# Kernel tuning notes

Measured on AMD Instinct MI355X. Metric: run time of the kernel, lower is better.

The kernel has to match this reference:

```python
import jax, jax.numpy as jnp
import numpy as np


def setup_inputs() -> dict:
    key = jax.random.key(0)
    k1, k2, k3 = jax.random.split(key, 3)
    N, Q, K, E = 8, 2048, 2048, 512
    query = jax.random.normal(k1, (N, Q, E), dtype=jnp.float32)
    keys = jax.random.normal(k2, (N, K, E), dtype=jnp.float32)
    values = jax.random.normal(k3, (N, K, E), dtype=jnp.float32)
    return {"query": query, "keys": keys, "values": values}


def reference(query, keys, values):
    # energy: [N, Q, K] -- note: NO 1/sqrt(d) scaling, matching the original
    energy = jnp.einsum('nqe,nke->nqk', query, keys)
    attention = jax.nn.softmax(energy, axis=-1)
    out = jnp.einsum('nqk,nke->nqe', attention, values)
    return out
```

## Files before the change

### kernel.cpp

```cpp
#include <hip/hip_runtime.h>
#include <stdint.h>


typedef __attribute__((ext_vector_type(8))) _Float16 half8;
typedef __attribute__((ext_vector_type(2))) _Float16 half2;
typedef __attribute__((ext_vector_type(4))) float    floatx4;

#define NBATCH 8
#define SEQ    2048
#define EDIM   512
static constexpr size_t NE = (size_t)NBATCH * SEQ * EDIM;

__device__ __forceinline__ void block_sync_lds() {
  asm volatile("s_waitcnt lgkmcnt(0)\n\ts_barrier" ::: "memory");
}

__device__ __forceinline__ half8 cvt8(float4 a, float4 b) {
  half8 h;
  h[0] = (_Float16)a.x; h[1] = (_Float16)a.y; h[2] = (_Float16)a.z; h[3] = (_Float16)a.w;
  h[4] = (_Float16)b.x; h[5] = (_Float16)b.y; h[6] = (_Float16)b.z; h[7] = (_Float16)b.w;
  return h;
}


__global__ void make_frags(const float* __restrict__ q, const float* __restrict__ k,
                           const float* __restrict__ v,
                           _Float16* __restrict__ qf, _Float16* __restrict__ kf,
                           _Float16* __restrict__ vf) {
  __shared__ float lds[32][260];
  const int tid = threadIdx.x;
  const int seg = blockIdx.x >> 9;
  const int b   = blockIdx.x & 511;
  const int n = b >> 6, kt = b & 63;
  const float* src = (seg == 0 ? q : seg == 1 ? k : v) + ((size_t)n * SEQ + kt * 32) * EDIM;

  if (seg < 2) {
    _Float16* dst = (seg == 0 ? qf : kf) + ((size_t)(n * 128 + kt * 2) * 16) * 512;
#pragma unroll
    for (int eh = 0; eh < 2; eh++) {
      if (eh) __syncthreads();
#pragma unroll
      for (int i = 0; i < 8; i++) {
        int c = i * 256 + tid;
        int row = c >> 6, col4 = c & 63;
        float4 x = *reinterpret_cast<const float4*>(src + (size_t)row * EDIM + eh * 256 + col4 * 4);
        *reinterpret_cast<float4*>(&lds[row][col4 * 4]) = x;
      }
      __syncthreads();
#pragma unroll
      for (int i = 0; i < 4; i++) {
        int fl = i * 256 + tid;
        int lane = fl & 63, idx = fl >> 6;
        int est_l = idx & 7, rt_l = idx >> 3;
        int m15 = lane & 15, q4 = lane >> 4;
        const float* p = &lds[rt_l * 16 + m15][est_l * 32 + q4 * 8];
        float4 a = *reinterpret_cast<const float4*>(p);
        float4 bb = *reinterpret_cast<const float4*>(p + 4);
        *reinterpret_cast<half8*>(dst + ((size_t)(rt_l * 16 + eh * 8 + est_l)) * 512 + lane * 8) =
            cvt8(a, bb);
      }
    }
  } else {
    _Float16* dst = vf + ((size_t)(n * 64 + kt) * 32) * 512;
#pragma unroll
    for (int eh = 0; eh < 2; eh++) {
      if (eh) __syncthreads();
#pragma unroll
      for (int i = 0; i < 8; i++) {
        int c = i * 256 + tid;
        int row = c >> 6, col4 = c & 63;
        float4 x = *reinterpret_cast<const float4*>(src + (size_t)row * EDIM + eh * 256 + col4 * 4);
        *reinterpret_cast<float4*>(&lds[row][col4 * 4]) = x;
      }
      __syncthreads();
#pragma unroll
      for (int i = 0; i < 4; i++) {
        int fl = i * 256 + tid;
        int etl = fl >> 6, ln = fl & 63;
        int m15 = ln & 15, q4 = ln >> 4;
        int e_local = etl * 16 + m15;
        half8 h;
#pragma unroll
        for (int j = 0; j < 8; j++) h[j] = (_Float16)lds[q4 * 8 + j][e_local];
        *reinterpret_cast<half8*>(dst + ((size_t)eh * 1024 + fl) * 8) = h;
      }
    }
  }
}

__launch_bounds__(512, 4)
__global__ void attn_fused(const _Float16* __restrict__ qf, const _Float16* __restrict__ kf,
                           const _Float16* __restrict__ vf, float* __restrict__ out) {
  __shared__ float    s_part[4][32][36];
  __shared__ _Float16 p_lds[32][40];
  __shared__ float    m_lds[32], l_lds[32], a_lds[32];

  const int tid  = threadIdx.x;
  const int lane = tid & 63, w = tid >> 6;
  const int m15  = lane & 15, q4 = lane >> 4;
  const int n    = blockIdx.x & 7, qt = blockIdx.x >> 3;
  const int ks   = w & 1, es = w >> 1;

  if (tid < 32) { m_lds[tid] = -3.0e38f; l_lds[tid] = 0.0f; }

  half8 qfr[2][4];
  {
    const uint32_t qbase = ((uint32_t)(n * 128 + qt * 2) * 16 + es * 4) * 512 + (uint32_t)lane * 8;
#pragma unroll
    for (int s = 0; s < 2; s++)
#pragma unroll
      for (int i = 0; i < 4; i++)
        qfr[s][i] = *reinterpret_cast<const half8*>(qf + qbase + (uint32_t)(s * 16 + i) * 512);
  }

  floatx4 oacc[2][4];
#pragma unroll
  for (int s = 0; s < 2; s++)
#pragma unroll
    for (int j = 0; j < 4; j++) oacc[s][j] = (floatx4){0.f, 0.f, 0.f, 0.f};

  uint32_t koff = ((uint32_t)(n * 128 + ks) * 16 + es * 4) * 512 + (uint32_t)lane * 8;
  uint32_t voff = ((uint32_t)(n * 64) * 32 + w * 4) * 512 + (uint32_t)lane * 8;

  block_sync_lds();

  for (int t = 0; t < 64; t++) {
    half8 kfr[4];
#pragma unroll
    for (int i = 0; i < 4; i++)
      kfr[i] = *reinterpret_cast<const half8*>(kf + koff + (uint32_t)i * 512);
    koff += 16384;

    floatx4 sacc[2];
    sacc[0] = (floatx4){0.f, 0.f, 0.f, 0.f};
    sacc[1] = (floatx4){0.f, 0.f, 0.f, 0.f};
    __builtin_amdgcn_s_setprio(1);
#pragma unroll
    for (int i = 0; i < 4; i++) {
      sacc[0] = __builtin_amdgcn_mfma_f32_16x16x32_f16(qfr[0][i], kfr[i], sacc[0], 0, 0, 0);
      sacc[1] = __builtin_amdgcn_mfma_f32_16x16x32_f16(qfr[1][i], kfr[i], sacc[1], 0, 0, 0);
    }
    __builtin_amdgcn_s_setprio(0);

    half8 vfr[4];
#pragma unroll
    for (int j = 0; j < 4; j++)
      vfr[j] = *reinterpret_cast<const half8*>(vf + voff + (uint32_t)j * 512);
    voff += 16384;

#pragma unroll
    for (int s = 0; s < 2; s++)
#pragma unroll
      for (int r = 0; r < 4; r++)
        s_part[es][s * 16 + q4 * 4 + r][ks * 16 + m15] = sacc[s][r];
    block_sync_lds();

    {
      const int r = tid >> 4, sub = tid & 15, c = sub * 2;
      float svx = s_part[0][r][c],     svy = s_part[0][r][c + 1];
#pragma unroll
      for (int pl = 1; pl < 4; pl++) { svx += s_part[pl][r][c]; svy += s_part[pl][r][c + 1]; }
      float mx = fmaxf(svx, svy);
#pragma unroll
      for (int o = 1; o < 16; o <<= 1) mx = fmaxf(mx, __shfl_xor(mx, o));
      const float mo = m_lds[r];
      const float mn = fmaxf(mo, mx);
      const float px = __expf(svx - mn), py = __expf(svy - mn);
      float rs = px + py;
#pragma unroll
      for (int o = 1; o < 16; o <<= 1) rs += __shfl_xor(rs, o);
      if (sub == 0) {
        const float al = __expf(mo - mn);
        a_lds[r] = al; m_lds[r] = mn; l_lds[r] = l_lds[r] * al + rs;
      }
      half2 ph; ph[0] = (_Float16)px; ph[1] = (_Float16)py;
      *reinterpret_cast<half2*>(&p_lds[r][c]) = ph;
    }
    block_sync_lds();

    half8 pfr[2];
    pfr[0] = *reinterpret_cast<const half8*>(&p_lds[m15][q4 * 8]);
    pfr[1] = *reinterpret_cast<const half8*>(&p_lds[16 + m15][q4 * 8]);
    {
      floatx4 al0 = *reinterpret_cast<floatx4*>(&a_lds[q4 * 4]);
      floatx4 al1 = *reinterpret_cast<floatx4*>(&a_lds[16 + q4 * 4]);
#pragma unroll
      for (int j = 0; j < 4; j++) { oacc[0][j] *= al0; oacc[1][j] *= al1; }
    }
    __builtin_amdgcn_s_setprio(1);
#pragma unroll
    for (int j = 0; j < 4; j++) {
      oacc[0][j] = __builtin_amdgcn_mfma_f32_16x16x32_f16(pfr[0], vfr[j], oacc[0][j], 0, 0, 0);
      oacc[1][j] = __builtin_amdgcn_mfma_f32_16x16x32_f16(pfr[1], vfr[j], oacc[1][j], 0, 0, 0);
    }
    __builtin_amdgcn_s_setprio(0);
  }

  const int q0 = qt * 32;
#pragma unroll
  for (int s = 0; s < 2; s++) {
    floatx4 lv = *reinterpret_cast<floatx4*>(&l_lds[s * 16 + q4 * 4]);
#pragma unroll
    for (int j = 0; j < 4; j++) {
      const int col = (w * 4 + j) * 16 + m15;
#pragma unroll
      for (int r = 0; r < 4; r++) {
        const int row = s * 16 + q4 * 4 + r;
        out[((size_t)n * SEQ + q0 + row) * EDIM + col] = oacc[s][j][r] / lv[r];
      }
    }
  }
}

__global__ void attn_fallback(const float* __restrict__ q, const float* __restrict__ k,
                              const float* __restrict__ v, float* __restrict__ out) {
  __shared__ float qrow[EDIM];
  __shared__ float sc[SEQ];
  __shared__ float red[16];
  const int tid = threadIdx.x;
  const int n = blockIdx.x >> 11, qi = blockIdx.x & 2047;
  const int wv = tid >> 6, ln = tid & 63;
  const float* qp = q + ((size_t)n * SEQ + qi) * EDIM;
  for (int e = tid; e < EDIM; e += 256) qrow[e] = qp[e];
  __syncthreads();
  for (int kk = wv; kk < SEQ; kk += 4) {
    const float* kp = k + ((size_t)n * SEQ + kk) * EDIM;
    float s = 0.f;
    for (int e = ln; e < EDIM; e += 64) s = fmaf(qrow[e], kp[e], s);
    for (int o = 32; o > 0; o >>= 1) s += __shfl_down(s, o);
    if (ln == 0) sc[kk] = s;
  }
  __syncthreads();
  float mx = -3.0e38f;
  for (int kk = tid; kk < SEQ; kk += 256) mx = fmaxf(mx, sc[kk]);
  for (int o = 32; o > 0; o >>= 1) mx = fmaxf(mx, __shfl_down(mx, o));
  if (ln == 0) red[wv] = mx;
  __syncthreads();
  if (tid == 0) {
    float m2 = red[0];
    for (int i = 1; i < 4; i++) m2 = fmaxf(m2, red[i]);
    red[8] = m2;
  }
  __syncthreads();
  const float m = red[8];
  float ls = 0.f;
  for (int kk = tid; kk < SEQ; kk += 256) { float p = __expf(sc[kk] - m); sc[kk] = p; ls += p; }
  for (int o = 32; o > 0; o >>= 1) ls += __shfl_down(ls, o);
  if (ln == 0) red[wv] = ls;
  __syncthreads();
  if (tid == 0) { red[9] = red[0] + red[1] + red[2] + red[3]; }
  __syncthreads();
  const float linv = 1.f / red[9];
  for (int e = tid; e < EDIM; e += 256) {
    float acc = 0.f;
    const float* vp = v + ((size_t)n * SEQ) * EDIM + e;
    for (int kk = 0; kk < SEQ; kk++) acc = fmaf(sc[kk], vp[(size_t)kk * EDIM], acc);
    out[((size_t)n * SEQ + qi) * EDIM + e] = acc * linv;
  }
}

extern "C" void kernel_launch(void* const* d_in, const int* in_sizes, int n_in,
                              void* d_out, int out_size, void* d_ws, size_t ws_size,
                              hipStream_t stream) {
  const float* q = (const float*)d_in[0];
  const float* k = (const float*)d_in[1];
  const float* v = (const float*)d_in[2];
  float* out = (float*)d_out;
  const size_t need = 3 * NE * sizeof(_Float16);
  if (ws_size >= need) {
    _Float16* qf = (_Float16*)d_ws;
    _Float16* kf = qf + NE;
    _Float16* vf = kf + NE;
    make_frags<<<1536, 256, 0, stream>>>(q, k, v, qf, kf, vf);
    attn_fused<<<512, 512, 0, stream>>>(qf, kf, vf, out);
  } else {
    attn_fallback<<<16384, 256, 0, stream>>>(q, k, v, out);
  }
}
```

Before: 239.1 us.

## Convert Q in-kernel instead of prepass, and prefetch next K fragments

New measurement: 234.9 us. Within noise of the previous version (-1.8%).

```diff
diff --git a/kernel.cpp b/kernel.cpp
--- a/kernel.cpp
+++ b/kernel.cpp
@@ -23,19 +23,17 @@
 }
 
 
-__global__ void make_frags(const float* __restrict__ q, const float* __restrict__ k,
-                           const float* __restrict__ v,
-                           _Float16* __restrict__ qf, _Float16* __restrict__ kf,
-                           _Float16* __restrict__ vf) {
+__global__ void make_frags(const float* __restrict__ k, const float* __restrict__ v,
+                           _Float16* __restrict__ kf, _Float16* __restrict__ vf) {
   __shared__ float lds[32][260];
   const int tid = threadIdx.x;
   const int seg = blockIdx.x >> 9;
   const int b   = blockIdx.x & 511;
   const int n = b >> 6, kt = b & 63;
-  const float* src = (seg == 0 ? q : seg == 1 ? k : v) + ((size_t)n * SEQ + kt * 32) * EDIM;
-
-  if (seg < 2) {
-    _Float16* dst = (seg == 0 ? qf : kf) + ((size_t)(n * 128 + kt * 2) * 16) * 512;
+  const float* src = (seg == 0 ? k : v) + ((size_t)n * SEQ + kt * 32) * EDIM;
+
+  if (seg == 0) {
+    _Float16* dst = kf + ((size_t)(n * 128 + kt * 2) * 16) * 512;
 #pragma unroll
     for (int eh = 0; eh < 2; eh++) {
       if (eh) __syncthreads();
@@ -89,7 +87,7 @@
 }
 
 __launch_bounds__(512, 4)
-__global__ void attn_fused(const _Float16* __restrict__ qf, const _Float16* __restrict__ kf,
+__global__ void attn_fused(const float* __restrict__ q, const _Float16* __restrict__ kf,
                            const _Float16* __restrict__ vf, float* __restrict__ out) {
   __shared__ float    s_part[4][32][36];
   __shared__ _Float16 p_lds[32][40];
@@ -105,12 +103,16 @@
 
   half8 qfr[2][4];
   {
-    const uint32_t qbase = ((uint32_t)(n * 128 + qt * 2) * 16 + es * 4) * 512 + (uint32_t)lane * 8;
+    const float* qb = q + ((size_t)n * SEQ + qt * 32 + m15) * EDIM + es * 128 + q4 * 8;
 #pragma unroll
     for (int s = 0; s < 2; s++)
 #pragma unroll
-      for (int i = 0; i < 4; i++)
-        qfr[s][i] = *reinterpret_cast<const half8*>(qf + qbase + (uint32_t)(s * 16 + i) * 512);
+      for (int i = 0; i < 4; i++) {
+        const float* src = qb + (size_t)s * 16 * EDIM + i * 32;
+        float4 a = *reinterpret_cast<const float4*>(src);
+        float4 b = *reinterpret_cast<const float4*>(src + 4);
+        qfr[s][i] = cvt8(a, b);
+      }
   }
 
   floatx4 oacc[2][4];
@@ -122,25 +124,31 @@
   uint32_t koff = ((uint32_t)(n * 128 + ks) * 16 + es * 4) * 512 + (uint32_t)lane * 8;
   uint32_t voff = ((uint32_t)(n * 64) * 32 + w * 4) * 512 + (uint32_t)lane * 8;
 
+  half8 kcur[4];
+#pragma unroll
+  for (int i = 0; i < 4; i++)
+    kcur[i] = *reinterpret_cast<const half8*>(kf + koff + (uint32_t)i * 512);
+  koff += 16384;
+
   block_sync_lds();
 
   for (int t = 0; t < 64; t++) {
-    half8 kfr[4];
-#pragma unroll
-    for (int i = 0; i < 4; i++)
-      kfr[i] = *reinterpret_cast<const half8*>(kf + koff + (uint32_t)i * 512);
-    koff += 16384;
-
     floatx4 sacc[2];
     sacc[0] = (floatx4){0.f, 0.f, 0.f, 0.f};
     sacc[1] = (floatx4){0.f, 0.f, 0.f, 0.f};
     __builtin_amdgcn_s_setprio(1);
 #pragma unroll
     for (int i = 0; i < 4; i++) {
-      sacc[0] = __builtin_amdgcn_mfma_f32_16x16x32_f16(qfr[0][i], kfr[i], sacc[0], 0, 0, 0);
-      sacc[1] = __builtin_amdgcn_mfma_f32_16x16x32_f16(qfr[1][i], kfr[i], sacc[1], 0, 0, 0);
+      sacc[0] = __builtin_amdgcn_mfma_f32_16x16x32_f16(qfr[0][i], kcur[i], sacc[0], 0, 0, 0);
+      sacc[1] = __builtin_amdgcn_mfma_f32_16x16x32_f16(qfr[1][i], kcur[i], sacc[1], 0, 0, 0);
     }
     __builtin_amdgcn_s_setprio(0);
+
+    half8 knxt[4];
+#pragma unroll
+    for (int i = 0; i < 4; i++)
+      knxt[i] = *reinterpret_cast<const half8*>(kf + koff + (uint32_t)i * 512);
+    koff += 16384;
 
     half8 vfr[4];
 #pragma unroll
@@ -194,6 +202,9 @@
       oacc[1][j] = __builtin_amdgcn_mfma_f32_16x16x32_f16(pfr[1], vfr[j], oacc[1][j], 0, 0, 0);
     }
     __builtin_amdgcn_s_setprio(0);
+
+#pragma unroll
+    for (int i = 0; i < 4; i++) kcur[i] = knxt[i];
   }
 
   const int q0 = qt * 32;
@@ -266,13 +277,12 @@
   const float* k = (const float*)d_in[1];
   const float* v = (const float*)d_in[2];
   float* out = (float*)d_out;
-  const size_t need = 3 * NE * sizeof(_Float16);
+  const size_t need = 2 * NE * sizeof(_Float16);
   if (ws_size >= need) {
-    _Float16* qf = (_Float16*)d_ws;
-    _Float16* kf = qf + NE;
+    _Float16* kf = (_Float16*)d_ws;
     _Float16* vf = kf + NE;
-    make_frags<<<1536, 256, 0, stream>>>(q, k, v, qf, kf, vf);
-    attn_fused<<<512, 512, 0, stream>>>(qf, kf, vf, out);
+    make_frags<<<1024, 256, 0, stream>>>(k, v, kf, vf);
+    attn_fused<<<512, 512, 0, stream>>>(q, kf, vf, out);
   } else {
     attn_fallback<<<16384, 256, 0, stream>>>(q, k, v, out);
   }
```

## Fuse fragment conversion and attention into one cooperative kernel with grid sync

Applied to the files above, without the earlier changes.

After: 320.5 us. 34.1% more time.

```diff
diff --git a/kernel.cpp b/kernel.cpp
--- a/kernel.cpp
+++ b/kernel.cpp
@@ -1,5 +1,8 @@
 #include <hip/hip_runtime.h>
+#include <hip/hip_cooperative_groups.h>
 #include <stdint.h>
+
+namespace cg = cooperative_groups;
 
 
 typedef __attribute__((ext_vector_type(8))) _Float16 half8;
@@ -22,6 +25,191 @@
   return h;
 }
 
+
+__launch_bounds__(512, 4)
+__global__ void attn_all(const float* __restrict__ q, const float* __restrict__ k,
+                         const float* __restrict__ v,
+                         _Float16* __restrict__ qf, _Float16* __restrict__ kf,
+                         _Float16* __restrict__ vf, float* __restrict__ out) {
+  __shared__ __align__(16) char smem[33280];
+
+  const int tid = threadIdx.x;
+
+  {
+    float (*lds)[260] = reinterpret_cast<float (*)[260]>(smem);
+    const int b = blockIdx.x;
+    const int n = b >> 6, kt = b & 63;
+#pragma unroll 1
+    for (int seg = 0; seg < 3; seg++) {
+      const float* src = (seg == 0 ? q : seg == 1 ? k : v) +
+                         ((size_t)n * SEQ + kt * 32) * EDIM;
+      if (seg) __syncthreads();
+#pragma unroll 1
+      for (int eh = 0; eh < 2; eh++) {
+        if (eh) __syncthreads();
+#pragma unroll
+        for (int i = 0; i < 4; i++) {
+          int c = i * 512 + tid;
+          int row = c >> 6, col4 = c & 63;
+          float4 x = *reinterpret_cast<const float4*>(src + (size_t)row * EDIM + eh * 256 + col4 * 4);
+          *reinterpret_cast<float4*>(&lds[row][col4 * 4]) = x;
+        }
+        __syncthreads();
+        if (seg < 2) {
+          _Float16* dst = (seg == 0 ? qf : kf) + ((size_t)(n * 128 + kt * 2) * 16) * 512;
+#pragma unroll
+          for (int i = 0; i < 2; i++) {
+            int fl = i * 512 + tid;
+            int lane = fl & 63, idx = fl >> 6;
+            int est_l = idx & 7, rt_l = idx >> 3;
+            int m15 = lane & 15, q4 = lane >> 4;
+            const float* p = &lds[rt_l * 16 + m15][est_l * 32 + q4 * 8];
+            float4 a = *reinterpret_cast<const float4*>(p);
+            float4 bb = *reinterpret_cast<const float4*>(p + 4);
+            *reinterpret_cast<half8*>(dst + ((size_t)(rt_l * 16 + eh * 8 + est_l)) * 512 + lane * 8) =
+                cvt8(a, bb);
+          }
+        } else {
+          _Float16* dst = vf + ((size_t)(n * 64 + kt) * 32) * 512;
+#pragma unroll
+          for (int i = 0; i < 2; i++) {
+            int fl = i * 512 + tid;
+            int etl = fl >> 6, ln = fl & 63;
+            int m15 = ln & 15, q4 = ln >> 4;
+            int e_local = etl * 16 + m15;
+            half8 h;
+#pragma unroll
+            for (int j = 0; j < 8; j++) h[j] = (_Float16)lds[q4 * 8 + j][e_local];
+            *reinterpret_cast<half8*>(dst + ((size_t)eh * 1024 + fl) * 8) = h;
+          }
+        }
+      }
+    }
+  }
+
+  cg::this_grid().sync();
+
+  float    (*s_part)[32][36] = reinterpret_cast<float (*)[32][36]>(smem);
+  _Float16 (*p_lds)[40]      = reinterpret_cast<_Float16 (*)[40]>(smem + 18432);
+  float*    m_lds            = reinterpret_cast<float*>(smem + 18432 + 2560);
+  float*    l_lds            = m_lds + 32;
+  float*    a_lds            = m_lds + 64;
+
+  const int lane = tid & 63, w = tid >> 6;
+  const int m15  = lane & 15, q4 = lane >> 4;
+  const int n    = blockIdx.x & 7, qt = blockIdx.x >> 3;
+  const int ks   = w & 1, es = w >> 1;
+
+  if (tid < 32) { m_lds[tid] = -3.0e38f; l_lds[tid] = 0.0f; }
+
+  half8 qfr[2][4];
+  {
+    const uint32_t qbase = ((uint32_t)(n * 128 + qt * 2) * 16 + es * 4) * 512 + (uint32_t)lane * 8;
+#pragma unroll
+    for (int s = 0; s < 2; s++)
+#pragma unroll
+      for (int i = 0; i < 4; i++)
+        qfr[s][i] = *reinterpret_cast<const half8*>(qf + qbase + (uint32_t)(s * 16 + i) * 512);
+  }
+
+  floatx4 oacc[2][4];
+#pragma unroll
+  for (int s = 0; s < 2; s++)
+#pragma unroll
+    for (int j = 0; j < 4; j++) oacc[s][j] = (floatx4){0.f, 0.f, 0.f, 0.f};
+
+  uint32_t koff = ((uint32_t)(n * 128 + ks) * 16 + es * 4) * 512 + (uint32_t)lane * 8;
+  uint32_t voff = ((uint32_t)(n * 64) * 32 + w * 4) * 512 + (uint32_t)lane * 8;
+
+  block_sync_lds();
+
+  for (int t = 0; t < 64; t++) {
+    half8 kfr[4];
+#pragma unroll
+    for (int i = 0; i < 4; i++)
+      kfr[i] = *reinterpret_cast<const half8*>(kf + koff + (uint32_t)i * 512);
+    koff += 16384;
+
+    floatx4 sacc[2];
+    sacc[0] = (floatx4){0.f, 0.f, 0.f, 0.f};
+    sacc[1] = (floatx4){0.f, 0.f, 0.f, 0.f};
+    __builtin_amdgcn_s_setprio(1);
+#pragma unroll
+    for (int i = 0; i < 4; i++) {
+      sacc[0] = __builtin_amdgcn_mfma_f32_16x16x32_f16(qfr[0][i], kfr[i], sacc[0], 0, 0, 0);
+      sacc[1] = __builtin_amdgcn_mfma_f32_16x16x32_f16(qfr[1][i], kfr[i], sacc[1], 0, 0, 0);
+    }
+    __builtin_amdgcn_s_setprio(0);
+
+    half8 vfr[4];
+#pragma unroll
+    for (int j = 0; j < 4; j++)
+      vfr[j] = *reinterpret_cast<const half8*>(vf + voff + (uint32_t)j * 512);
+    voff += 16384;
+
+#pragma unroll
+    for (int s = 0; s < 2; s++)
+#pragma unroll
+      for (int r = 0; r < 4; r++)
+        s_part[es][s * 16 + q4 * 4 + r][ks * 16 + m15] = sacc[s][r];
+    block_sync_lds();
+
+    {
+      const int r = tid >> 4, sub = tid & 15, c = sub * 2;
+      float svx = s_part[0][r][c],     svy = s_part[0][r][c + 1];
+#pragma unroll
+      for (int pl = 1; pl < 4; pl++) { svx += s_part[pl][r][c]; svy += s_part[pl][r][c + 1]; }
+      float mx = fmaxf(svx, svy);
+#pragma unroll
+      for (int o = 1; o < 16; o <<= 1) mx = fmaxf(mx, __shfl_xor(mx, o));
+      const float mo = m_lds[r];
+      const float mn = fmaxf(mo, mx);
+      const float px = __expf(svx - mn), py = __expf(svy - mn);
+      float rs = px + py;
+#pragma unroll
+      for (int o = 1; o < 16; o <<= 1) rs += __shfl_xor(rs, o);
+      if (sub == 0) {
+        const float al = __expf(mo - mn);
+        a_lds[r] = al; m_lds[r] = mn; l_lds[r] = l_lds[r] * al + rs;
+      }
+      half2 ph; ph[0] = (_Float16)px; ph[1] = (_Float16)py;
+      *reinterpret_cast<half2*>(&p_lds[r][c]) = ph;
+    }
+    block_sync_lds();
+
+    half8 pfr[2];
+    pfr[0] = *reinterpret_cast<const half8*>(&p_lds[m15][q4 * 8]);
+    pfr[1] = *reinterpret_cast<const half8*>(&p_lds[16 + m15][q4 * 8]);
+    {
+      floatx4 al0 = *reinterpret_cast<floatx4*>(&a_lds[q4 * 4]);
+      floatx4 al1 = *reinterpret_cast<floatx4*>(&a_lds[16 + q4 * 4]);
+#pragma unroll
+      for (int j = 0; j < 4; j++) { oacc[0][j] *= al0; oacc[1][j] *= al1; }
+    }
+    __builtin_amdgcn_s_setprio(1);
+#pragma unroll
+    for (int j = 0; j < 4; j++) {
+      oacc[0][j] = __builtin_amdgcn_mfma_f32_16x16x32_f16(pfr[0], vfr[j], oacc[0][j], 0, 0, 0);
+      oacc[1][j] = __builtin_amdgcn_mfma_f32_16x16x32_f16(pfr[1], vfr[j], oacc[1][j], 0, 0, 0);
+    }
+    __builtin_amdgcn_s_setprio(0);
+  }
+
+  const int q0 = qt * 32;
+#pragma unroll
+  for (int s = 0; s < 2; s++) {
+    floatx4 lv = *reinterpret_cast<floatx4*>(&l_lds[s * 16 + q4 * 4]);
+#pragma unroll
+    for (int j = 0; j < 4; j++) {
+      const int col = (w * 4 + j) * 16 + m15;
+#pragma unroll
+      for (int r = 0; r < 4; r++) {
+        const int row = s * 16 + q4 * 4 + r;
+        out[((size_t)n * SEQ + q0 + row) * EDIM + col] = oacc[s][j][r] / lv[r];
+      }
+    }
+  }
+}
 
 __global__ void make_frags(const float* __restrict__ q, const float* __restrict__ k,
                            const float* __restrict__ v,
@@ -271,8 +459,14 @@
     _Float16* qf = (_Float16*)d_ws;
     _Float16* kf = qf + NE;
     _Float16* vf = kf + NE;
-    make_frags<<<1536, 256, 0, stream>>>(q, k, v, qf, kf, vf);
-    attn_fused<<<512, 512, 0, stream>>>(qf, kf, vf, out);
+    void* args[] = {(void*)&q, (void*)&k, (void*)&v,
+                    (void*)&qf, (void*)&kf, (void*)&vf, (void*)&out};
+    hipError_t err = hipLaunchCooperativeKernel(
+        reinterpret_cast<void*>(attn_all), dim3(512), dim3(512), args, 0, stream);
+    if (err != hipSuccess) {
+      make_frags<<<1536, 256, 0, stream>>>(q, k, v, qf, kf, vf);
+      attn_fused<<<512, 512, 0, stream>>>(qf, kf, vf, out);
+    }
   } else {
     attn_fallback<<<16384, 256, 0, stream>>>(q, k, v, out);
   }
```
